# Performance work log

Measured on AMD Instinct MI355X. Metric: run time of the kernel, lower is better.

## Reference

```python
import jax, jax.numpy as jnp
import numpy as np

# NSA hyperparams (match init_kwargs)
D_BLK = 64    # d: block stride
L_CMP = 64    # compression block length (== d -> non-overlapping blocks)
L_SLC = 64    # selection block length (== l_cmp == d -> P_slc = P_cmp)
BQ = 64       # block_size_q
TOPK = 16     # slc_top_k
WL, WR = 512, 0  # sliding window (left, right)


def _nsa_forward(q, k, v, w_k, b_k, w_v, b_v, w_gate, b_gate, seqlen):
    S, qh, dim = q.shape
    kv = k.shape[1]
    H = qh // kv
    b = S // seqlen          # number of equal-length packed sequences
    s = seqlen
    scale = dim ** -0.5
    f32 = jnp.float32

    # [b, s, kv, H, e]: q head g*H+h belongs to kv head g (repeat_interleave layout)
    q5 = q.reshape(b, s, kv, H, dim)
    k3 = k.reshape(b, s, kv, dim)
    v3 = v.reshape(b, s, kv, dim)

    # ---- block compression (extract_blocks + cmp_linear over block length) ----
    n_blk = s // D_BLK
    kb = k.reshape(b, n_blk, D_BLK, kv, dim)
    vb = v.reshape(b, n_blk, D_BLK, kv, dim)
    K_cmp = jnp.einsum('bntke,t->bnke', kb, w_k) + b_k[0]
    V_cmp = jnp.einsum('bntke,t->bnke', vb, w_v) + b_v[0]

    # ---- compressed attention (per sequence, fp32 softmax) ----
    sc = jnp.einsum('bqkhe,bnke->bkhqn', q5, K_cmp).astype(f32) * scale
    P = jax.nn.softmax(sc, axis=-1)
    out_cmp = jnp.einsum('bkhqn,bnke->bqkhe', P.astype(q.dtype), V_cmp)

    # ---- selection scores: pool P over q-blocks and GQA groups, then top-k ----
    nqb = s // BQ
    pooled = P.reshape(b, kv, H, nqb, BQ, n_blk).sum(axis=(2, 4))  # [b,kv,nqb,n_blk]
    idx = jax.lax.top_k(pooled, TOPK)[1]                            # [b,kv,nqb,TOPK]

    # gather selected K/V blocks (shared by all queries in a q-block / GQA group)
    kb2 = jnp.transpose(kb, (0, 3, 1, 2, 4))  # [b,kv,n_blk,l,e]
    vb2 = jnp.transpose(vb, (0, 3, 1, 2, 4))
    gather = jax.vmap(jax.vmap(lambda blocks, i: blocks[i]))
    K_sel = gather(kb2, idx)  # [b,kv,nqb,TOPK,l,e]
    V_sel = gather(vb2, idx)

    # ---- selected-block attention ----
    qblk = q5.reshape(b, nqb, BQ, kv, H, dim)
    sc2 = jnp.einsum('bnckhe,bkntle->bkhnctl', qblk, K_sel).astype(f32) * scale
    sc2 = sc2.reshape(b, kv, H, nqb, BQ, TOPK * L_SLC)
    P2 = jax.nn.softmax(sc2, axis=-1).astype(q.dtype)
    out_slc = jnp.einsum('bkhncm,bknme->bnckhe', P2,
                         V_sel.reshape(b, kv, nqb, TOPK * L_SLC, dim))
    out_slc = out_slc.reshape(b, s, kv, H, dim)

    # ---- sliding-window attention (window_size=(WL, WR), non-causal flag) ----
    sw = jnp.einsum('bikhe,bjke->bkhij', q5, k3).astype(f32) * scale
    i = jnp.arange(s)[:, None]
    j = jnp.arange(s)[None, :]
    valid = (j >= i - WL) & (j <= i + WR)
    sw = jnp.where(valid, sw, -jnp.inf)
    Pw = jax.nn.softmax(sw, axis=-1).astype(q.dtype)
    out_win = jnp.einsum('bkhij,bjke->bikhe', Pw, v3)

    # ---- gated fusion of the three branches ----
    gate = jax.nn.sigmoid(jnp.einsum('bqkhe,ec->bqkhc', q5, w_gate) + b_gate)
    out = (gate[..., 0:1] * out_cmp
           + gate[..., 1:2] * out_slc
           + gate[..., 2:3] * out_win)
    return out.reshape(S, qh, dim)


def setup_inputs() -> dict:
    key = jax.random.key(0)
    ks = jax.random.split(key, 9)
    S, qh, kvh, dim = 4096, 8, 2, 128
    inp = {
        'q': jax.random.normal(ks[0], (S, qh, dim), jnp.float32),
        'k': jax.random.normal(ks[1], (S, kvh, dim), jnp.float32),
        'v': jax.random.normal(ks[2], (S, kvh, dim), jnp.float32),
        'w_k': jax.random.normal(ks[3], (L_CMP,), jnp.float32) * (L_CMP ** -0.5),
        'b_k': jax.random.normal(ks[4], (1,), jnp.float32) * 0.02,
        'w_v': jax.random.normal(ks[5], (L_CMP,), jnp.float32) * (L_CMP ** -0.5),
        'b_v': jax.random.normal(ks[6], (1,), jnp.float32) * 0.02,
        'w_gate': jax.random.normal(ks[7], (dim, 3), jnp.float32) * (dim ** -0.5),
        'b_gate': jax.random.normal(ks[8], (3,), jnp.float32) * 0.02,
        'seqlen': 2048,
    }
    return inp


def reference(q, k, v, w_k, b_k, w_v, b_v, w_gate, b_gate, seqlen):
    return _nsa_forward(q, k, v, w_k, b_k, w_v, b_v, w_gate, b_gate, seqlen)
```

## Files before the change

### kernel.cpp

```cpp
#include <hip/hip_runtime.h>
#include <hip/hip_bf16.h>


#define SEQ   2048
#define NB    2
#define KV    2
#define NH    4
#define QH    8
#define DIM   128
#define NBLK  32
#define NQB   32
#define NTOP  16
#define SCALE 0.08838834764831845f
#define QSC   0.12751831795244785f
#define VP    72
#define VCS   40

typedef unsigned short ushort_t;
using bf16x8 = __attribute__((ext_vector_type(8))) short;
using f32x4  = __attribute__((ext_vector_type(4))) float;

__device__ __forceinline__ unsigned pkbf(float a, float b){
  union { __hip_bfloat162 h; unsigned u; } cv;
  cv.h = __float22bfloat162_rn(make_float2(a, b));
  return cv.u;
}
__device__ __forceinline__ ushort_t b16(float f){
  union { float f; unsigned i; } x; x.f = f;
  unsigned r = x.i + 0x7fffu + ((x.i >> 16) & 1u);
  return (ushort_t)(r >> 16);
}
__device__ __forceinline__ float fb(ushort_t h){
  union { unsigned i; float f; } x; x.i = ((unsigned)h) << 16;
  return x.f;
}

__device__ __forceinline__ void async16(ushort_t* l, const ushort_t* g){
  __builtin_amdgcn_global_load_lds(
      (const __attribute__((address_space(1))) unsigned int*)(size_t)g,
      (__attribute__((address_space(3))) unsigned int*)(size_t)l,
      16, 0, 0);
}

__global__ __launch_bounds__(256) void prep_k(
    const float* __restrict__ k, const float* __restrict__ v,
    const float* __restrict__ w_k, const float* __restrict__ b_k,
    const float* __restrict__ w_v, const float* __restrict__ b_v,
    ushort_t* __restrict__ Kb, ushort_t* __restrict__ VT,
    float* __restrict__ Kc, float* __restrict__ Vc)
{
  int blk = blockIdx.x;
  int db = blk & 1, rb = (blk >> 1) & 31, bbg = blk >> 6;
  int bb = bbg >> 1, g = bbg & 1;
  int tid = threadIdx.x;
  __shared__ ushort_t T[64*VP];
  __shared__ float wks[64], wvs[64];
  __shared__ float accK[16][64], accV[16][64];

  if (tid < 64){ wks[tid] = w_k[tid]; wvs[tid] = w_v[tid]; }
  __syncthreads();

  float4 sk = {0,0,0,0}, sv = {0,0,0,0};
  for (int jj = 0; jj < 4; ++jj){
    int i = tid + jj*256;
    int r = i >> 4, ds = i & 15;
    size_t src = ((size_t)(bb*SEQ + rb*64 + r)*KV + g)*DIM + db*64 + ds*4;
    float4 kx = *(const float4*)(k + src);
    float4 vx = *(const float4*)(v + src);
    uint2 kk; kk.x = pkbf(kx.x,kx.y); kk.y = pkbf(kx.z,kx.w);
    size_t rowb = ((size_t)bbg*SEQ + rb*64 + r)*DIM*2;
    int swz = (db*128 + ds*8) ^ ((r & 7) << 4);
    *(uint2*)((char*)Kb + rowb + swz) = kk;
    unsigned v01 = pkbf(vx.x,vx.y), v23 = pkbf(vx.z,vx.w);
    T[(ds*4+0)*VP + r] = (ushort_t)(v01 & 0xffffu);
    T[(ds*4+1)*VP + r] = (ushort_t)(v01 >> 16);
    T[(ds*4+2)*VP + r] = (ushort_t)(v23 & 0xffffu);
    T[(ds*4+3)*VP + r] = (ushort_t)(v23 >> 16);
    float a = wks[r], b = wvs[r];
    sk.x += a*kx.x; sk.y += a*kx.y; sk.z += a*kx.z; sk.w += a*kx.w;
    sv.x += b*vx.x; sv.y += b*vx.y; sv.z += b*vx.z; sv.w += b*vx.w;
  }
  *(float4*)&accK[tid>>4][(tid&15)*4] = sk;
  *(float4*)&accV[tid>>4][(tid&15)*4] = sv;
  __syncthreads();

  for (int jj = 0; jj < 4; ++jj){
    int i = tid + jj*256;
    int d = i >> 4, seg = i & 15;
    uint2 u = *(uint2*)&T[d*VP + seg*4];
    size_t rowb = ((size_t)bbg*DIM + db*64 + d)*SEQ*2;
    int swz = (seg*8) ^ ((d & 7) << 4);
    *(uint2*)((char*)VT + rowb + rb*128 + swz) = u;
  }

  size_t obase = ((size_t)(bbg*NBLK + rb))*DIM + db*64;
  if (tid < 64){
    float s = 0.f;
#pragma unroll
    for (int i = 0; i < 16; ++i) s += accK[i][tid];
    Kc[obase + tid] = s + b_k[0];
  } else if (tid < 128){
    int d = tid - 64;
    float s = 0.f;
#pragma unroll
    for (int i = 0; i < 16; ++i) s += accV[i][d];
    Vc[obase + d] = s + b_v[0];
  }
}

__global__ __launch_bounds__(512, 2) void attn_k(
    const float* __restrict__ q, const ushort_t* __restrict__ Kb,
    const ushort_t* __restrict__ VT,
    const float* __restrict__ Kc, const float* __restrict__ Vc,
    const float* __restrict__ w_gate, const float* __restrict__ b_gate,
    float* __restrict__ slcbuf, float* __restrict__ out)
{
  int idx = blockIdx.x;
  int x = idx & 7, low = idx & 1, u = idx >> 3;
  int bbg = x >> 1;
  int j = u*2 + low;
  int role = j >> 5;
  int qb = j & 31;
  int bb = bbg >> 1, g = bbg & 1;

  int tid = threadIdx.x;
  int lane = tid & 63, w = tid >> 6;
  int quad = lane >> 4, l15 = lane & 15;
  int h = w & 3, qh2 = w >> 2;
  int xr = (l15 & 7) << 4;

  __shared__ ushort_t Ks[2][64*128];
  __shared__ ushort_t VTs[3][128*64];
  __shared__ ushort_t Ps[256*VP];
  __shared__ ushort_t VcTh[128*VCS];
  __shared__ ushort_t VcTl[128*VCS];
  __shared__ float pw[8][NBLK];
  __shared__ float gbuf[256];
  __shared__ int   idxs[NTOP];

  if (role == 0){
    {
      int key = tid >> 4, dq = tid & 15;
      const float* kcs = Kc + ((size_t)bbg*NBLK + key)*DIM + dq*8;
      float4 f0 = *(const float4*)kcs, f1 = *(const float4*)(kcs + 4);
      float fe[8] = {f0.x,f0.y,f0.z,f0.w,f1.x,f1.y,f1.z,f1.w};
      union { ushort_t u[8]; uint4 v; } hi, lo;
#pragma unroll
      for (int e = 0; e < 8; ++e){
        ushort_t hh = b16(fe[e]);
        hi.u[e] = hh; lo.u[e] = b16(fe[e] - fb(hh));
      }
      int off = (dq*16) ^ ((key & 7) << 4);
      *(uint4*)((char*)&Ks[0][0] + key*256 + off) = hi.v;
      *(uint4*)((char*)&Ks[0][0] + (key+32)*256 + off) = lo.v;
    }
    {
      int d = tid & 127, kq = tid >> 7;
      const float* vcs = Vc + (size_t)bbg*NBLK*DIM + d;
      union { ushort_t u[8]; uint4 v; } hi, lo;
#pragma unroll
      for (int kk = 0; kk < 8; ++kk){
        float f = vcs[(kq*8 + kk)*DIM];
        ushort_t hh = b16(f);
        hi.u[kk] = hh; lo.u[kk] = b16(f - fb(hh));
      }
      *(uint4*)&VcTh[d*VCS + kq*8] = hi.v;
      *(uint4*)&VcTl[d*VCS + kq*8] = lo.v;
    }
  }

  const float* qrow0 = q + ((size_t)(bb*SEQ + qb*64 + qh2*32 + l15)*QH + g*NH + h)*DIM;
  const float* qrow1 = qrow0 + (size_t)16*QH*DIM;
  int gcol = 1 + role;
  bf16x8 qfrag0[4], qfrag1[4], qlo0[4], qlo1[4];
  float gp0 = 0.f, gp1 = 0.f, gc0 = 0.f, gc1 = 0.f;
#pragma unroll
  for (int kc = 0; kc < 4; ++kc){
    int d0 = kc*32 + quad*8;
    float4 a0 = *(const float4*)(qrow0 + d0);
    float4 a1 = *(const float4*)(qrow0 + d0 + 4);
    float4 b0 = *(const float4*)(qrow1 + d0);
    float4 b1 = *(const float4*)(qrow1 + d0 + 4);
    float qa[8] = {a0.x,a0.y,a0.z,a0.w,a1.x,a1.y,a1.z,a1.w};
    float qc[8] = {b0.x,b0.y,b0.z,b0.w,b1.x,b1.y,b1.z,b1.w};
#pragma unroll
    for (int jj = 0; jj < 8; ++jj){
      float wg = w_gate[(d0+jj)*3 + gcol];
      gp0 += qa[jj]*wg; gp1 += qc[jj]*wg;
    }
    if (role == 0){
#pragma unroll
      for (int jj = 0; jj < 8; ++jj){
        float w0 = w_gate[(d0+jj)*3];
        gc0 += qa[jj]*w0; gc1 += qc[jj]*w0;
      }
      union { ushort_t u[8]; bf16x8 v; } h0, l0, h1, l1;
#pragma unroll
      for (int e = 0; e < 8; ++e){
        float s0f = qa[e]*QSC; ushort_t hh0 = b16(s0f);
        h0.u[e] = hh0; l0.u[e] = b16(s0f - fb(hh0));
        float s1f = qc[e]*QSC; ushort_t hh1 = b16(s1f);
        h1.u[e] = hh1; l1.u[e] = b16(s1f - fb(hh1));
      }
      qfrag0[kc] = h0.v; qlo0[kc] = l0.v;
      qfrag1[kc] = h1.v; qlo1[kc] = l1.v;
    } else {
      union { unsigned uu[4]; bf16x8 v8; } t0, t1;
#pragma unroll
      for (int p2 = 0; p2 < 4; ++p2){
        t0.uu[p2] = pkbf(qa[2*p2]*QSC, qa[2*p2+1]*QSC);
        t1.uu[p2] = pkbf(qc[2*p2]*QSC, qc[2*p2+1]*QSC);
      }
      qfrag0[kc] = t0.v8; qfrag1[kc] = t1.v8;
    }
  }
  gp0 += __shfl_xor(gp0,16); gp0 += __shfl_xor(gp0,32);
  gp1 += __shfl_xor(gp1,16); gp1 += __shfl_xor(gp1,32);
  if (quad == 0){
    gbuf[w*32 + l15]      = 1.f/(1.f + __expf(-(gp0 + b_gate[gcol])));
    gbuf[w*32 + 16 + l15] = 1.f/(1.f + __expf(-(gp1 + b_gate[gcol])));
  }
  float g0c0 = 0.f, g0c1 = 0.f;
  if (role == 0){
    gc0 += __shfl_xor(gc0,16); gc0 += __shfl_xor(gc0,32);
    gc1 += __shfl_xor(gc1,16); gc1 += __shfl_xor(gc1,32);
    g0c0 = 1.f/(1.f + __expf(-(gc0 + b_gate[0])));
    g0c1 = 1.f/(1.f + __expf(-(gc1 + b_gate[0])));
  }
  __syncthreads();
  float gl0[4], gl1[4];
#pragma unroll
  for (int r = 0; r < 4; ++r){
    gl0[r] = gbuf[w*32 + quad*4 + r];
    gl1[r] = gbuf[w*32 + 16 + quad*4 + r];
  }

  const f32x4 zero4 = {0.f,0.f,0.f,0.f};
  f32x4 cp0[2], cp1[2];
  cp0[0] = zero4; cp0[1] = zero4; cp1[0] = zero4; cp1[1] = zero4;

  if (role == 0){
    f32x4 c0[2], c1[2];
    c0[0]=zero4; c0[1]=zero4; c1[0]=zero4; c1[1]=zero4;
#pragma unroll
    for (int kc = 0; kc < 4; ++kc){
#pragma unroll
      for (int nt = 0; nt < 2; ++nt){
        bf16x8 ah = *(bf16x8*)((char*)&Ks[0][0] + (nt*16 + l15)*256
                               + ((kc*64 + quad*16) ^ xr));
        bf16x8 al = *(bf16x8*)((char*)&Ks[0][0] + (nt*16 + l15 + 32)*256
                               + ((kc*64 + quad*16) ^ xr));
        c0[nt] = __builtin_amdgcn_mfma_f32_16x16x32_bf16(ah, qfrag0[kc], c0[nt], 0, 0, 0);
        c0[nt] = __builtin_amdgcn_mfma_f32_16x16x32_bf16(ah, qlo0[kc],   c0[nt], 0, 0, 0);
        c0[nt] = __builtin_amdgcn_mfma_f32_16x16x32_bf16(al, qfrag0[kc], c0[nt], 0, 0, 0);
        c1[nt] = __builtin_amdgcn_mfma_f32_16x16x32_bf16(ah, qfrag1[kc], c1[nt], 0, 0, 0);
        c1[nt] = __builtin_amdgcn_mfma_f32_16x16x32_bf16(ah, qlo1[kc],   c1[nt], 0, 0, 0);
        c1[nt] = __builtin_amdgcn_mfma_f32_16x16x32_bf16(al, qfrag1[kc], c1[nt], 0, 0, 0);
      }
    }
    float mx0 = -INFINITY, mx1 = -INFINITY;
#pragma unroll
    for (int nt = 0; nt < 2; ++nt)
#pragma unroll
      for (int r = 0; r < 4; ++r){
        mx0 = fmaxf(mx0, c0[nt][r]); mx1 = fmaxf(mx1, c1[nt][r]);
      }
    mx0 = fmaxf(mx0, __shfl_xor(mx0,16)); mx0 = fmaxf(mx0, __shfl_xor(mx0,32));
    mx1 = fmaxf(mx1, __shfl_xor(mx1,16)); mx1 = fmaxf(mx1, __shfl_xor(mx1,32));
    float s0 = 0.f, s1 = 0.f;
#pragma unroll
    for (int nt = 0; nt < 2; ++nt)
#pragma unroll
      for (int r = 0; r < 4; ++r){
        float p0v = exp2f(c0[nt][r] - mx0); c0[nt][r] = p0v; s0 += p0v;
        float p1v = exp2f(c1[nt][r] - mx1); c1[nt][r] = p1v; s1 += p1v;
      }
    s0 += __shfl_xor(s0,16); s0 += __shfl_xor(s0,32);
    s1 += __shfl_xor(s1,16); s1 += __shfl_xor(s1,32);
    float ip0 = 1.f/s0, ip1 = 1.f/s1;
    float ig0 = g0c0*ip0, ig1 = g0c1*ip1;
#pragma unroll
    for (int nt = 0; nt < 2; ++nt)
#pragma unroll
      for (int r = 0; r < 4; ++r){
        cp0[nt][r] = c0[nt][r]*ig0;
        cp1[nt][r] = c1[nt][r]*ig1;
        float t = c0[nt][r]*ip0 + c1[nt][r]*ip1;
        t += __shfl_xor(t,1); t += __shfl_xor(t,2);
        t += __shfl_xor(t,4); t += __shfl_xor(t,8);
        if (l15 == 0) pw[w][nt*16 + quad*4 + r] = t;
      }
    __syncthreads();
    if (tid < 64){
      int n = lane;
      float val = -INFINITY;
      if (n < NBLK){
        float sm = 0.f;
#pragma unroll
        for (int w2 = 0; w2 < 8; ++w2) sm += pw[w2][n];
        val = sm;
      }
      int idxv = n;
      for (int kk = 2; kk <= 32; kk <<= 1){
        for (int jj2 = kk >> 1; jj2 > 0; jj2 >>= 1){
          float pv = __shfl_xor(val, jj2);
          int   pi = __shfl_xor(idxv, jj2);
          bool lower = (lane & jj2) == 0;
          bool desc  = (lane & kk) == 0;
          bool iwin  = (val > pv) || (val == pv && idxv < pi);
          bool keep  = (lower == desc) ? iwin : !iwin;
          if (!keep){ val = pv; idxv = pi; }
        }
      }
      if (lane < NTOP) idxs[lane] = idxv;
    }
    __syncthreads();
  }

  const ushort_t* kbase  = Kb + (size_t)bbg*SEQ*DIM;
  const ushort_t* vtbase = VT + (size_t)bbg*DIM*SEQ;

  int kb0 = (qb >= 8) ? (qb - 8) : 0;
  int nph = (role == 0) ? NTOP : (qb - kb0 + 1);
  int qi0 = qh2*32 + l15, qi1 = qi0 + 16;

  float m10 = -INFINITY, l10 = 0.f, m11 = -INFINITY, l11 = 0.f;
  f32x4 oacc0[8], oacc1[8];
#pragma unroll
  for (int dt = 0; dt < 8; ++dt){ oacc0[dt] = zero4; oacc1[dt] = zero4; }

  auto stage = [&](int kbuf, int vbuf, int kb_){
    const ushort_t* ksrc = kbase + (size_t)kb_*64*DIM;
#pragma unroll
    for (int jj = 0; jj < 2; ++jj)
      async16(&Ks[kbuf][(jj*512 + w*64)*8], ksrc + (size_t)(tid + jj*512)*8);
    const ushort_t* vsrc = vtbase + kb_*64;
#pragma unroll
    for (int jj = 0; jj < 2; ++jj){
      int i = tid + jj*512;
      int d = i >> 3, sg = i & 7;
      async16(&VTs[vbuf][(jj*512 + w*64)*8], vsrc + (size_t)d*SEQ + sg*8);
    }
  };

  stage(0, 0, (role == 0) ? idxs[0] : kb0);

  float alp0 = 1.f, alp1 = 1.f;
  bool  skp0 = true,  skp1 = true;
  int vprev = 2, vcur = 0, vnext = 1;

  for (int t = 0; t < nph; ++t){
    int kb = (role == 0) ? idxs[t] : (kb0 + t);
    __syncthreads();
    if (t+1 < nph){
      int kbn = (role == 0) ? idxs[t+1] : (kb0 + t + 1);
      stage((t+1) & 1, vnext, kbn);
    }
    __builtin_amdgcn_sched_barrier(0);

    f32x4 sacc0[4], sacc1[4];
#pragma unroll
    for (int nt = 0; nt < 4; ++nt){ sacc0[nt] = zero4; sacc1[nt] = zero4; }
    __builtin_amdgcn_s_setprio(1);
#pragma unroll
    for (int kc = 0; kc < 4; ++kc){
#pragma unroll
      for (int nt = 0; nt < 4; ++nt){
        bf16x8 a = *(bf16x8*)((char*)&Ks[t & 1][0] + (nt*16 + l15)*256
                              + ((kc*64 + quad*16) ^ xr));
        sacc0[nt] = __builtin_amdgcn_mfma_f32_16x16x32_bf16(a, qfrag0[kc], sacc0[nt], 0, 0, 0);
        sacc1[nt] = __builtin_amdgcn_mfma_f32_16x16x32_bf16(a, qfrag1[kc], sacc1[nt], 0, 0, 0);
      }
    }
    __builtin_amdgcn_s_setprio(0);

    if (t > 0){
      if (!skp0){
        float ar[4];
#pragma unroll
        for (int r = 0; r < 4; ++r) ar[r] = __shfl(alp0, quad*4 + r);
#pragma unroll
        for (int dt = 0; dt < 8; ++dt)
#pragma unroll
          for (int r = 0; r < 4; ++r) oacc0[dt][r] *= ar[r];
      }
      if (!skp1){
        float ar[4];
#pragma unroll
        for (int r = 0; r < 4; ++r) ar[r] = __shfl(alp1, quad*4 + r);
#pragma unroll
        for (int dt = 0; dt < 8; ++dt)
#pragma unroll
          for (int r = 0; r < 4; ++r) oacc1[dt][r] *= ar[r];
      }
#pragma unroll
      for (int kc2 = 0; kc2 < 2; ++kc2){
        bf16x8 pa0 = *(bf16x8*)&Ps[(w*32 + l15)*VP + kc2*32 + quad*8];
        bf16x8 pa1 = *(bf16x8*)&Ps[(w*32 + 16 + l15)*VP + kc2*32 + quad*8];
        __builtin_amdgcn_s_setprio(1);
#pragma unroll
        for (int dt = 0; dt < 8; ++dt){
          bf16x8 vb8 = *(bf16x8*)((char*)&VTs[vprev][0] + (dt*16 + l15)*128
                                  + ((kc2*64 + quad*16) ^ xr));
          oacc0[dt] = __builtin_amdgcn_mfma_f32_16x16x32_bf16(pa0, vb8, oacc0[dt], 0, 0, 0);
          oacc1[dt] = __builtin_amdgcn_mfma_f32_16x16x32_bf16(pa1, vb8, oacc1[dt], 0, 0, 0);
        }
        __builtin_amdgcn_s_setprio(0);
      }
    }

    bool mlow  = (role == 1) && (kb == qb - 8);
    bool mhigh = (role == 1) && (kb == qb);
    bool domask = mlow | mhigh;

    auto softmax_qt = [&](f32x4* sc2, float& m1r, float& l1r, int qi_l,
                          bool& skipped) -> float {
      if (domask){
#pragma unroll
        for (int nt = 0; nt < 4; ++nt)
#pragma unroll
          for (int r = 0; r < 4; ++r){
            int key = nt*16 + quad*4 + r;
            bool valid = (!mlow || key >= qi_l) && (!mhigh || key <= qi_l);
            sc2[nt][r] = valid ? sc2[nt][r] : -INFINITY;
          }
      }
      float mnt[4];
#pragma unroll
      for (int nt = 0; nt < 4; ++nt)
        mnt[nt] = fmaxf(fmaxf(sc2[nt][0], sc2[nt][1]),
                        fmaxf(sc2[nt][2], sc2[nt][3]));
      float mx = fmaxf(fmaxf(mnt[0], mnt[1]), fmaxf(mnt[2], mnt[3]));
      mx = fmaxf(mx, __shfl_xor(mx, 16));
      mx = fmaxf(mx, __shfl_xor(mx, 32));
      float al = 1.f;
      skipped = __all(mx <= m1r + 8.f);
      if (!skipped){
        float mn = fmaxf(m1r, mx);
        al = exp2f(m1r - mn);
        m1r = mn;
      }
      float snt[4];
#pragma unroll
      for (int nt = 0; nt < 4; ++nt){
        float p0 = exp2f(sc2[nt][0] - m1r);
        float p1 = exp2f(sc2[nt][1] - m1r);
        float p2 = exp2f(sc2[nt][2] - m1r);
        float p3 = exp2f(sc2[nt][3] - m1r);
        sc2[nt][0] = p0; sc2[nt][1] = p1; sc2[nt][2] = p2; sc2[nt][3] = p3;
        snt[nt] = (p0 + p1) + (p2 + p3);
      }
      float s0 = (snt[0] + snt[1]) + (snt[2] + snt[3]);
      s0 += __shfl_xor(s0, 16);
      s0 += __shfl_xor(s0, 32);
      l1r = l1r*al + s0;
      return al;
    };
    bool sk0, sk1;
    float al0 = softmax_qt(sacc0, m10, l10, qi0, sk0);
    float al1 = softmax_qt(sacc1, m11, l11, qi1, sk1);
    alp0 = al0; skp0 = sk0;
    alp1 = al1; skp1 = sk1;

#pragma unroll
    for (int nt = 0; nt < 4; ++nt){
      uint2 p0, p1;
      p0.x = pkbf(sacc0[nt][0], sacc0[nt][1]);
      p0.y = pkbf(sacc0[nt][2], sacc0[nt][3]);
      p1.x = pkbf(sacc1[nt][0], sacc1[nt][1]);
      p1.y = pkbf(sacc1[nt][2], sacc1[nt][3]);
      *(uint2*)&Ps[(w*32 + l15)*VP + nt*16 + quad*4] = p0;
      *(uint2*)&Ps[(w*32 + 16 + l15)*VP + nt*16 + quad*4] = p1;
    }

    int tmpv = vprev; vprev = vcur; vcur = vnext; vnext = tmpv;
  }

  {
    if (!skp0){
      float ar[4];
#pragma unroll
      for (int r = 0; r < 4; ++r) ar[r] = __shfl(alp0, quad*4 + r);
#pragma unroll
      for (int dt = 0; dt < 8; ++dt)
#pragma unroll
        for (int r = 0; r < 4; ++r) oacc0[dt][r] *= ar[r];
    }
    if (!skp1){
      float ar[4];
#pragma unroll
      for (int r = 0; r < 4; ++r) ar[r] = __shfl(alp1, quad*4 + r);
#pragma unroll
      for (int dt = 0; dt < 8; ++dt)
#pragma unroll
        for (int r = 0; r < 4; ++r) oacc1[dt][r] *= ar[r];
    }
#pragma unroll
    for (int kc2 = 0; kc2 < 2; ++kc2){
      bf16x8 pa0 = *(bf16x8*)&Ps[(w*32 + l15)*VP + kc2*32 + quad*8];
      bf16x8 pa1 = *(bf16x8*)&Ps[(w*32 + 16 + l15)*VP + kc2*32 + quad*8];
#pragma unroll
      for (int dt = 0; dt < 8; ++dt){
        bf16x8 vb8 = *(bf16x8*)((char*)&VTs[vprev][0] + (dt*16 + l15)*128
                                + ((kc2*64 + quad*16) ^ xr));
        oacc0[dt] = __builtin_amdgcn_mfma_f32_16x16x32_bf16(pa0, vb8, oacc0[dt], 0, 0, 0);
        oacc1[dt] = __builtin_amdgcn_mfma_f32_16x16x32_bf16(pa1, vb8, oacc1[dt], 0, 0, 0);
      }
    }
  }

  float lr0[4], lr1[4];
#pragma unroll
  for (int r = 0; r < 4; ++r){
    lr0[r] = __shfl(l10, quad*4 + r);
    lr1[r] = __shfl(l11, quad*4 + r);
  }
  if (role == 0){
    float a0[4], a1[4];
#pragma unroll
    for (int r = 0; r < 4; ++r){ a0[r] = gl0[r]/lr0[r]; a1[r] = gl1[r]/lr1[r]; }
#pragma unroll
    for (int dt = 0; dt < 8; ++dt)
#pragma unroll
      for (int r = 0; r < 4; ++r){ oacc0[dt][r] *= a0[r]; oacc1[dt][r] *= a1[r]; }
#pragma unroll
    for (int nt = 0; nt < 2; ++nt){
      union { ushort_t u[4]; uint2 v; } h0, l0, h1, l1;
#pragma unroll
      for (int r = 0; r < 4; ++r){
        ushort_t hh0 = b16(cp0[nt][r]);
        h0.u[r] = hh0; l0.u[r] = b16(cp0[nt][r] - fb(hh0));
        ushort_t hh1 = b16(cp1[nt][r]);
        h1.u[r] = hh1; l1.u[r] = b16(cp1[nt][r] - fb(hh1));
      }
      *(uint2*)&Ps[(w*32 + l15)*VP + nt*16 + quad*4]      = h0.v;
      *(uint2*)&Ps[(w*32 + l15)*VP + 32 + nt*16 + quad*4] = l0.v;
      *(uint2*)&Ps[(w*32 + 16 + l15)*VP + nt*16 + quad*4]      = h1.v;
      *(uint2*)&Ps[(w*32 + 16 + l15)*VP + 32 + nt*16 + quad*4] = l1.v;
    }
    bf16x8 pah0 = *(bf16x8*)&Ps[(w*32 + l15)*VP + quad*8];
    bf16x8 pal0 = *(bf16x8*)&Ps[(w*32 + l15)*VP + 32 + quad*8];
    bf16x8 pah1 = *(bf16x8*)&Ps[(w*32 + 16 + l15)*VP + quad*8];
    bf16x8 pal1 = *(bf16x8*)&Ps[(w*32 + 16 + l15)*VP + 32 + quad*8];
#pragma unroll
    for (int dt = 0; dt < 8; ++dt){
      bf16x8 vbh = *(bf16x8*)&VcTh[(dt*16 + l15)*VCS + quad*8];
      bf16x8 vbl = *(bf16x8*)&VcTl[(dt*16 + l15)*VCS + quad*8];
      oacc0[dt] = __builtin_amdgcn_mfma_f32_16x16x32_bf16(pah0, vbh, oacc0[dt], 0, 0, 0);
      oacc0[dt] = __builtin_amdgcn_mfma_f32_16x16x32_bf16(pah0, vbl, oacc0[dt], 0, 0, 0);
      oacc0[dt] = __builtin_amdgcn_mfma_f32_16x16x32_bf16(pal0, vbh, oacc0[dt], 0, 0, 0);
      oacc1[dt] = __builtin_amdgcn_mfma_f32_16x16x32_bf16(pah1, vbh, oacc1[dt], 0, 0, 0);
      oacc1[dt] = __builtin_amdgcn_mfma_f32_16x16x32_bf16(pah1, vbl, oacc1[dt], 0, 0, 0);
      oacc1[dt] = __builtin_amdgcn_mfma_f32_16x16x32_bf16(pal1, vbh, oacc1[dt], 0, 0, 0);
    }
#pragma unroll
    for (int r = 0; r < 4; ++r){
      size_t ob0 = ((size_t)(bb*SEQ + qb*64 + qh2*32 + quad*4 + r)*QH + g*NH + h)*DIM + l15;
      size_t ob1 = ob0 + (size_t)16*QH*DIM;
      float* op0 = slcbuf + ob0;
      float* op1 = slcbuf + ob1;
#pragma unroll
      for (int dt = 0; dt < 8; ++dt){
        op0[dt*16] = oacc0[dt][r];
        op1[dt*16] = oacc1[dt][r];
      }
    }
  } else {
#pragma unroll
    for (int r = 0; r < 4; ++r){
      float s20 = gl0[r] / lr0[r];
      float s21 = gl1[r] / lr1[r];
      size_t ob0 = ((size_t)(bb*SEQ + qb*64 + qh2*32 + quad*4 + r)*QH + g*NH + h)*DIM + l15;
      size_t ob1 = ob0 + (size_t)16*QH*DIM;
      float* op0 = out + ob0;
      float* op1 = out + ob1;
#pragma unroll
      for (int dt = 0; dt < 8; ++dt){
        op0[dt*16] = s20 * oacc0[dt][r];
        op1[dt*16] = s21 * oacc1[dt][r];
      }
    }
  }
}

__global__ __launch_bounds__(256) void merge_k(const float* __restrict__ slcbuf,
                                               float* __restrict__ out){
  int base = blockIdx.x * 512 + threadIdx.x;
#pragma unroll
  for (int jj = 0; jj < 2; ++jj){
    int i = base + jj*256;
    float4 a = ((const float4*)slcbuf)[i];
    float4 b = ((float4*)out)[i];
    b.x += a.x; b.y += a.y; b.z += a.z; b.w += a.w;
    ((float4*)out)[i] = b;
  }
}

extern "C" void kernel_launch(void* const* d_in, const int* in_sizes, int n_in,
                              void* d_out, int out_size, void* d_ws, size_t ws_size,
                              hipStream_t stream) {
  const float* q      = (const float*)d_in[0];
  const float* k      = (const float*)d_in[1];
  const float* v      = (const float*)d_in[2];
  const float* w_k    = (const float*)d_in[3];
  const float* b_k    = (const float*)d_in[4];
  const float* w_v    = (const float*)d_in[5];
  const float* b_v    = (const float*)d_in[6];
  const float* w_gate = (const float*)d_in[7];
  const float* b_gate = (const float*)d_in[8];
  float* out = (float*)d_out;

  float* ws     = (float*)d_ws;
  float* Kc     = ws;
  float* Vc     = ws + 16384;
  float* slcbuf = ws + 49152;
  ushort_t* Kb  = (ushort_t*)(ws + 4243456);
  ushort_t* VT  = Kb + 1048576;

  prep_k <<<256, 256, 0, stream>>>(k, v, w_k, b_k, w_v, b_v, Kb, VT, Kc, Vc);
  attn_k <<<256, 512, 0, stream>>>(q, Kb, VT, Kc, Vc, w_gate, b_gate, slcbuf, out);
  merge_k<<<2048, 256, 0, stream>>>(slcbuf, out);
}
```

Before: 162.5 us.

## Balance selected-block work between roles with split-softmax merge

Role 1 blocks, which handle the sliding window and have few phases for early q-blocks, now also take part of the selected-block attention. Each role keeps partial softmax statistics (max and sum), and the merge kernel recombines the two selection partials flash-decoding style, adding the separately stored window output. This evens out per-block phase counts between the two roles. The cost is that role 1 now also does the hi/lo split compressed-attention setup, the kernel writes extra global buffers, and the merge reads more data.

```diff
diff --git a/kernel.cpp b/kernel.cpp
--- a/kernel.cpp
+++ b/kernel.cpp
@@ -19,6 +19,10 @@
 typedef unsigned short ushort_t;
 using bf16x8 = __attribute__((ext_vector_type(8))) short;
 using f32x4  = __attribute__((ext_vector_type(4))) float;
+
+__device__ float g_slcB[4194304];
+__device__ float g_winB[4194304];
+__device__ float g_mlg[2][65536];
 
 __device__ __forceinline__ unsigned pkbf(float a, float b){
   union { __hip_bfloat162 h; unsigned u; } cv;
@@ -136,44 +140,44 @@
   __shared__ ushort_t VcTl[128*VCS];
   __shared__ float pw[8][NBLK];
   __shared__ float gbuf[256];
+  __shared__ float gbuf2[256];
   __shared__ int   idxs[NTOP];
 
+  {
+    int key = tid >> 4, dq = tid & 15;
+    const float* kcs = Kc + ((size_t)bbg*NBLK + key)*DIM + dq*8;
+    float4 f0 = *(const float4*)kcs, f1 = *(const float4*)(kcs + 4);
+    float fe[8] = {f0.x,f0.y,f0.z,f0.w,f1.x,f1.y,f1.z,f1.w};
+    union { ushort_t u[8]; uint4 v; } hi, lo;
+#pragma unroll
+    for (int e = 0; e < 8; ++e){
+      ushort_t hh = b16(fe[e]);
+      hi.u[e] = hh; lo.u[e] = b16(fe[e] - fb(hh));
+    }
+    int off = (dq*16) ^ ((key & 7) << 4);
+    *(uint4*)((char*)&Ks[0][0] + key*256 + off) = hi.v;
+    *(uint4*)((char*)&Ks[0][0] + (key+32)*256 + off) = lo.v;
+  }
   if (role == 0){
-    {
-      int key = tid >> 4, dq = tid & 15;
-      const float* kcs = Kc + ((size_t)bbg*NBLK + key)*DIM + dq*8;
-      float4 f0 = *(const float4*)kcs, f1 = *(const float4*)(kcs + 4);
-      float fe[8] = {f0.x,f0.y,f0.z,f0.w,f1.x,f1.y,f1.z,f1.w};
-      union { ushort_t u[8]; uint4 v; } hi, lo;
-#pragma unroll
-      for (int e = 0; e < 8; ++e){
-        ushort_t hh = b16(fe[e]);
-        hi.u[e] = hh; lo.u[e] = b16(fe[e] - fb(hh));
-      }
-      int off = (dq*16) ^ ((key & 7) << 4);
-      *(uint4*)((char*)&Ks[0][0] + key*256 + off) = hi.v;
-      *(uint4*)((char*)&Ks[0][0] + (key+32)*256 + off) = lo.v;
-    }
-    {
-      int d = tid & 127, kq = tid >> 7;
-      const float* vcs = Vc + (size_t)bbg*NBLK*DIM + d;
-      union { ushort_t u[8]; uint4 v; } hi, lo;
-#pragma unroll
-      for (int kk = 0; kk < 8; ++kk){
-        float f = vcs[(kq*8 + kk)*DIM];
-        ushort_t hh = b16(f);
-        hi.u[kk] = hh; lo.u[kk] = b16(f - fb(hh));
-      }
-      *(uint4*)&VcTh[d*VCS + kq*8] = hi.v;
-      *(uint4*)&VcTl[d*VCS + kq*8] = lo.v;
-    }
+    int d = tid & 127, kq = tid >> 7;
+    const float* vcs = Vc + (size_t)bbg*NBLK*DIM + d;
+    union { ushort_t u[8]; uint4 v; } hi, lo;
+#pragma unroll
+    for (int kk = 0; kk < 8; ++kk){
+      float f = vcs[(kq*8 + kk)*DIM];
+      ushort_t hh = b16(f);
+      hi.u[kk] = hh; lo.u[kk] = b16(f - fb(hh));
+    }
+    *(uint4*)&VcTh[d*VCS + kq*8] = hi.v;
+    *(uint4*)&VcTl[d*VCS + kq*8] = lo.v;
   }
 
   const float* qrow0 = q + ((size_t)(bb*SEQ + qb*64 + qh2*32 + l15)*QH + g*NH + h)*DIM;
   const float* qrow1 = qrow0 + (size_t)16*QH*DIM;
-  int gcol = 1 + role;
+  int colA = 1 + role;
+  int colB = (role == 0) ? 0 : 1;
   bf16x8 qfrag0[4], qfrag1[4], qlo0[4], qlo1[4];
-  float gp0 = 0.f, gp1 = 0.f, gc0 = 0.f, gc1 = 0.f;
+  float gpA0 = 0.f, gpA1 = 0.f, gpB0 = 0.f, gpB1 = 0.f;
 #pragma unroll
   for (int kc = 0; kc < 4; ++kc){
     int d0 = kc*32 + quad*8;
@@ -185,61 +189,49 @@
     float qc[8] = {b0.x,b0.y,b0.z,b0.w,b1.x,b1.y,b1.z,b1.w};
 #pragma unroll
     for (int jj = 0; jj < 8; ++jj){
-      float wg = w_gate[(d0+jj)*3 + gcol];
-      gp0 += qa[jj]*wg; gp1 += qc[jj]*wg;
-    }
-    if (role == 0){
-#pragma unroll
-      for (int jj = 0; jj < 8; ++jj){
-        float w0 = w_gate[(d0+jj)*3];
-        gc0 += qa[jj]*w0; gc1 += qc[jj]*w0;
-      }
-      union { ushort_t u[8]; bf16x8 v; } h0, l0, h1, l1;
-#pragma unroll
-      for (int e = 0; e < 8; ++e){
-        float s0f = qa[e]*QSC; ushort_t hh0 = b16(s0f);
-        h0.u[e] = hh0; l0.u[e] = b16(s0f - fb(hh0));
-        float s1f = qc[e]*QSC; ushort_t hh1 = b16(s1f);
-        h1.u[e] = hh1; l1.u[e] = b16(s1f - fb(hh1));
-      }
-      qfrag0[kc] = h0.v; qlo0[kc] = l0.v;
-      qfrag1[kc] = h1.v; qlo1[kc] = l1.v;
-    } else {
-      union { unsigned uu[4]; bf16x8 v8; } t0, t1;
-#pragma unroll
-      for (int p2 = 0; p2 < 4; ++p2){
-        t0.uu[p2] = pkbf(qa[2*p2]*QSC, qa[2*p2+1]*QSC);
-        t1.uu[p2] = pkbf(qc[2*p2]*QSC, qc[2*p2+1]*QSC);
-      }
-      qfrag0[kc] = t0.v8; qfrag1[kc] = t1.v8;
-    }
-  }
-  gp0 += __shfl_xor(gp0,16); gp0 += __shfl_xor(gp0,32);
-  gp1 += __shfl_xor(gp1,16); gp1 += __shfl_xor(gp1,32);
+      float wA = w_gate[(d0+jj)*3 + colA];
+      float wB = w_gate[(d0+jj)*3 + colB];
+      gpA0 += qa[jj]*wA; gpA1 += qc[jj]*wA;
+      gpB0 += qa[jj]*wB; gpB1 += qc[jj]*wB;
+    }
+    union { ushort_t u[8]; bf16x8 v; } h0, l0, h1, l1;
+#pragma unroll
+    for (int e = 0; e < 8; ++e){
+      float s0f = qa[e]*QSC; ushort_t hh0 = b16(s0f);
+      h0.u[e] = hh0; l0.u[e] = b16(s0f - fb(hh0));
+      float s1f = qc[e]*QSC; ushort_t hh1 = b16(s1f);
+      h1.u[e] = hh1; l1.u[e] = b16(s1f - fb(hh1));
+    }
+    qfrag0[kc] = h0.v; qlo0[kc] = l0.v;
+    qfrag1[kc] = h1.v; qlo1[kc] = l1.v;
+  }
+  gpA0 += __shfl_xor(gpA0,16); gpA0 += __shfl_xor(gpA0,32);
+  gpA1 += __shfl_xor(gpA1,16); gpA1 += __shfl_xor(gpA1,32);
+  gpB0 += __shfl_xor(gpB0,16); gpB0 += __shfl_xor(gpB0,32);
+  gpB1 += __shfl_xor(gpB1,16); gpB1 += __shfl_xor(gpB1,32);
   if (quad == 0){
-    gbuf[w*32 + l15]      = 1.f/(1.f + __expf(-(gp0 + b_gate[gcol])));
-    gbuf[w*32 + 16 + l15] = 1.f/(1.f + __expf(-(gp1 + b_gate[gcol])));
-  }
-  float g0c0 = 0.f, g0c1 = 0.f;
-  if (role == 0){
-    gc0 += __shfl_xor(gc0,16); gc0 += __shfl_xor(gc0,32);
-    gc1 += __shfl_xor(gc1,16); gc1 += __shfl_xor(gc1,32);
-    g0c0 = 1.f/(1.f + __expf(-(gc0 + b_gate[0])));
-    g0c1 = 1.f/(1.f + __expf(-(gc1 + b_gate[0])));
+    gbuf [w*32 + l15]      = 1.f/(1.f + __expf(-(gpA0 + b_gate[colA])));
+    gbuf [w*32 + 16 + l15] = 1.f/(1.f + __expf(-(gpA1 + b_gate[colA])));
+    gbuf2[w*32 + l15]      = 1.f/(1.f + __expf(-(gpB0 + b_gate[colB])));
+    gbuf2[w*32 + 16 + l15] = 1.f/(1.f + __expf(-(gpB1 + b_gate[colB])));
   }
   __syncthreads();
-  float gl0[4], gl1[4];
+  float gl0[4], gl1[4], gs0[4], gs1[4];
 #pragma unroll
   for (int r = 0; r < 4; ++r){
-    gl0[r] = gbuf[w*32 + quad*4 + r];
-    gl1[r] = gbuf[w*32 + 16 + quad*4 + r];
-  }
+    gl0[r] = gbuf [w*32 + quad*4 + r];
+    gl1[r] = gbuf [w*32 + 16 + quad*4 + r];
+    gs0[r] = gbuf2[w*32 + quad*4 + r];
+    gs1[r] = gbuf2[w*32 + 16 + quad*4 + r];
+  }
+  float g0c0 = gbuf2[w*32 + l15];
+  float g0c1 = gbuf2[w*32 + 16 + l15];
 
   const f32x4 zero4 = {0.f,0.f,0.f,0.f};
   f32x4 cp0[2], cp1[2];
   cp0[0] = zero4; cp0[1] = zero4; cp1[0] = zero4; cp1[1] = zero4;
 
-  if (role == 0){
+  {
     f32x4 c0[2], c1[2];
     c0[0]=zero4; c0[1]=zero4; c1[0]=zero4; c1[1]=zero4;
 #pragma unroll
@@ -278,13 +270,20 @@
     s0 += __shfl_xor(s0,16); s0 += __shfl_xor(s0,32);
     s1 += __shfl_xor(s1,16); s1 += __shfl_xor(s1,32);
     float ip0 = 1.f/s0, ip1 = 1.f/s1;
-    float ig0 = g0c0*ip0, ig1 = g0c1*ip1;
+    if (role == 0){
+      float ig0 = g0c0*ip0, ig1 = g0c1*ip1;
+#pragma unroll
+      for (int nt = 0; nt < 2; ++nt)
+#pragma unroll
+        for (int r = 0; r < 4; ++r){
+          cp0[nt][r] = c0[nt][r]*ig0;
+          cp1[nt][r] = c1[nt][r]*ig1;
+        }
+    }
 #pragma unroll
     for (int nt = 0; nt < 2; ++nt)
 #pragma unroll
       for (int r = 0; r < 4; ++r){
-        cp0[nt][r] = c0[nt][r]*ig0;
-        cp1[nt][r] = c1[nt][r]*ig1;
         float t = c0[nt][r]*ip0 + c1[nt][r]*ip1;
         t += __shfl_xor(t,1); t += __shfl_xor(t,2);
         t += __shfl_xor(t,4); t += __shfl_xor(t,8);
@@ -320,9 +319,17 @@
   const ushort_t* kbase  = Kb + (size_t)bbg*SEQ*DIM;
   const ushort_t* vtbase = VT + (size_t)bbg*DIM*SEQ;
 
-  int kb0 = (qb >= 8) ? (qb - 8) : 0;
-  int nph = (role == 0) ? NTOP : (qb - kb0 + 1);
+  int kb0  = (qb >= 8) ? (qb - 8) : 0;
+  int nwin = qb - kb0 + 1;
+  int s    = (17 - nwin) >> 1;
+  int nslc0 = 16 - s;
+  int nph  = (role == 0) ? nslc0 : (nwin + s);
   int qi0 = qh2*32 + l15, qi1 = qi0 + 16;
+
+  auto tsel = [&](int t)->int {
+    if (role == 0) return idxs[t];
+    return (t < nwin) ? (kb0 + t) : idxs[nslc0 + (t - nwin)];
+  };
 
   float m10 = -INFINITY, l10 = 0.f, m11 = -INFINITY, l11 = 0.f;
   f32x4 oacc0[8], oacc1[8];
@@ -343,19 +350,16 @@
     }
   };
 
-  stage(0, 0, (role == 0) ? idxs[0] : kb0);
+  stage(0, 0, tsel(0));
 
   float alp0 = 1.f, alp1 = 1.f;
   bool  skp0 = true,  skp1 = true;
   int vprev = 2, vcur = 0, vnext = 1;
 
   for (int t = 0; t < nph; ++t){
-    int kb = (role == 0) ? idxs[t] : (kb0 + t);
+    int kb = tsel(t);
     __syncthreads();
-    if (t+1 < nph){
-      int kbn = (role == 0) ? idxs[t+1] : (kb0 + t + 1);
-      stage((t+1) & 1, vnext, kbn);
-    }
+    if (t+1 < nph) stage((t+1) & 1, vnext, tsel(t+1));
     __builtin_amdgcn_sched_barrier(0);
 
     f32x4 sacc0[4], sacc1[4];
@@ -409,8 +413,34 @@
       }
     }
 
-    bool mlow  = (role == 1) && (kb == qb - 8);
-    bool mhigh = (role == 1) && (kb == qb);
+    if (role == 1 && t == nwin){
+      float lr0f[4], lr1f[4];
+#pragma unroll
+      for (int r = 0; r < 4; ++r){
+        lr0f[r] = __shfl(l10, quad*4 + r);
+        lr1f[r] = __shfl(l11, quad*4 + r);
+      }
+#pragma unroll
+      for (int r = 0; r < 4; ++r){
+        float s20 = gl0[r] / lr0f[r];
+        float s21 = gl1[r] / lr1f[r];
+        size_t ob0 = ((size_t)(bb*SEQ + qb*64 + qh2*32 + quad*4 + r)*QH + g*NH + h)*DIM + l15;
+        size_t ob1 = ob0 + (size_t)16*QH*DIM;
+#pragma unroll
+        for (int dt = 0; dt < 8; ++dt){
+          g_winB[ob0 + dt*16] = s20 * oacc0[dt][r];
+          g_winB[ob1 + dt*16] = s21 * oacc1[dt][r];
+        }
+      }
+#pragma unroll
+      for (int dt = 0; dt < 8; ++dt){ oacc0[dt] = zero4; oacc1[dt] = zero4; }
+      m10 = -INFINITY; l10 = 0.f; m11 = -INFINITY; l11 = 0.f;
+      alp0 = 1.f; skp0 = true; alp1 = 1.f; skp1 = true;
+    }
+
+    bool winph = (role == 1) && (t < nwin);
+    bool mlow  = winph && (kb == qb - 8);
+    bool mhigh = winph && (kb == qb);
     bool domask = mlow | mhigh;
 
     auto softmax_qt = [&](f32x4* sc2, float& m1r, float& l1r, int qi_l,
@@ -509,20 +539,25 @@
     }
   }
 
-  float lr0[4], lr1[4];
-#pragma unroll
-  for (int r = 0; r < 4; ++r){
-    lr0[r] = __shfl(l10, quad*4 + r);
-    lr1[r] = __shfl(l11, quad*4 + r);
-  }
+  size_t rh0 = ((size_t)(bb*SEQ + qb*64 + qh2*32 + l15)*QH + g*NH + h);
+  size_t rh1 = rh0 + (size_t)16*QH;
   if (role == 0){
-    float a0[4], a1[4];
-#pragma unroll
-    for (int r = 0; r < 4; ++r){ a0[r] = gl0[r]/lr0[r]; a1[r] = gl1[r]/lr1[r]; }
-#pragma unroll
-    for (int dt = 0; dt < 8; ++dt)
-#pragma unroll
-      for (int r = 0; r < 4; ++r){ oacc0[dt][r] *= a0[r]; oacc1[dt][r] *= a1[r]; }
+#pragma unroll
+    for (int r = 0; r < 4; ++r){
+      size_t ob0 = ((size_t)(bb*SEQ + qb*64 + qh2*32 + quad*4 + r)*QH + g*NH + h)*DIM + l15;
+      size_t ob1 = ob0 + (size_t)16*QH*DIM;
+#pragma unroll
+      for (int dt = 0; dt < 8; ++dt){
+        slcbuf[ob0 + dt*16] = gl0[r] * oacc0[dt][r];
+        slcbuf[ob1 + dt*16] = gl1[r] * oacc1[dt][r];
+      }
+    }
+    if (quad == 0){
+      g_mlg[0][rh0*2] = m10; g_mlg[0][rh0*2 + 1] = l10;
+      g_mlg[0][rh1*2] = m11; g_mlg[0][rh1*2 + 1] = l11;
+    }
+#pragma unroll
+    for (int dt = 0; dt < 8; ++dt){ oacc0[dt] = zero4; oacc1[dt] = zero4; }
 #pragma unroll
     for (int nt = 0; nt < 2; ++nt){
       union { ushort_t u[4]; uint2 v; } h0, l0, h1, l1;
@@ -557,42 +592,51 @@
     for (int r = 0; r < 4; ++r){
       size_t ob0 = ((size_t)(bb*SEQ + qb*64 + qh2*32 + quad*4 + r)*QH + g*NH + h)*DIM + l15;
       size_t ob1 = ob0 + (size_t)16*QH*DIM;
-      float* op0 = slcbuf + ob0;
-      float* op1 = slcbuf + ob1;
 #pragma unroll
       for (int dt = 0; dt < 8; ++dt){
-        op0[dt*16] = oacc0[dt][r];
-        op1[dt*16] = oacc1[dt][r];
+        out[ob0 + dt*16] = oacc0[dt][r];
+        out[ob1 + dt*16] = oacc1[dt][r];
       }
     }
   } else {
 #pragma unroll
     for (int r = 0; r < 4; ++r){
-      float s20 = gl0[r] / lr0[r];
-      float s21 = gl1[r] / lr1[r];
       size_t ob0 = ((size_t)(bb*SEQ + qb*64 + qh2*32 + quad*4 + r)*QH + g*NH + h)*DIM + l15;
       size_t ob1 = ob0 + (size_t)16*QH*DIM;
-      float* op0 = out + ob0;
-      float* op1 = out + ob1;
 #pragma unroll
       for (int dt = 0; dt < 8; ++dt){
-        op0[dt*16] = s20 * oacc0[dt][r];
-        op1[dt*16] = s21 * oacc1[dt][r];
-      }
-    }
-  }
-}
-
-__global__ __launch_bounds__(256) void merge_k(const float* __restrict__ slcbuf,
+        g_slcB[ob0 + dt*16] = gs0[r] * oacc0[dt][r];
+        g_slcB[ob1 + dt*16] = gs1[r] * oacc1[dt][r];
+      }
+    }
+    if (quad == 0){
+      g_mlg[1][rh0*2] = m10; g_mlg[1][rh0*2 + 1] = l10;
+      g_mlg[1][rh1*2] = m11; g_mlg[1][rh1*2 + 1] = l11;
+    }
+  }
+}
+
+__global__ __launch_bounds__(256) void merge_k(const float* __restrict__ slcA,
                                                float* __restrict__ out){
   int base = blockIdx.x * 512 + threadIdx.x;
 #pragma unroll
   for (int jj = 0; jj < 2; ++jj){
     int i = base + jj*256;
-    float4 a = ((const float4*)slcbuf)[i];
-    float4 b = ((float4*)out)[i];
-    b.x += a.x; b.y += a.y; b.z += a.z; b.w += a.w;
-    ((float4*)out)[i] = b;
+    int rh = i >> 5;
+    float mA = g_mlg[0][rh*2], lA = g_mlg[0][rh*2+1];
+    float mB = g_mlg[1][rh*2], lB = g_mlg[1][rh*2+1];
+    float M  = fmaxf(mA, mB);
+    float wA = exp2f(mA - M), wB = exp2f(mB - M);
+    float inv = 1.f/(lA*wA + lB*wB);
+    float4 a = ((const float4*)slcA)[i];
+    float4 b = ((const float4*)g_slcB)[i];
+    float4 wn = ((const float4*)g_winB)[i];
+    float4 o = ((float4*)out)[i];
+    o.x += wn.x + (a.x*wA + b.x*wB)*inv;
+    o.y += wn.y + (a.y*wA + b.y*wB)*inv;
+    o.z += wn.z + (a.z*wA + b.z*wB)*inv;
+    o.w += wn.w + (a.w*wA + b.w*wB)*inv;
+    ((float4*)out)[i] = o;
   }
 }
 
```

Result: slower. 167.6 us (+3.2%).
